# Kernel optimization log

Measured on AMD Instinct MI355X. Metric: run time of the kernel, lower is better.

## Reference

```python
import jax, jax.numpy as jnp
import numpy as np

T_STEPS, N, STATE, HID, ACT, C = 32, 64, 64, 128, 32, 96


def setup_inputs() -> dict:
    key = jax.random.key(0)
    ks = jax.random.split(key, 16)
    s = 0.05
    inp = {
        'x': jax.random.normal(ks[0], (T_STEPS, N, STATE), jnp.float32),
        'a': jax.random.normal(ks[1], (T_STEPS, N, ACT), jnp.float32),
        # GRU layer 0 (input state_dim) and layer 1 (input hidden_dim)
        'wih0': jax.random.normal(ks[2], (3 * HID, STATE), jnp.float32) * s,
        'whh0': jax.random.normal(ks[3], (3 * HID, HID), jnp.float32) * s,
        'bih0': jax.random.normal(ks[4], (3 * HID,), jnp.float32) * s,
        'bhh0': jax.random.normal(ks[5], (3 * HID,), jnp.float32) * s,
        'wih1': jax.random.normal(ks[6], (3 * HID, HID), jnp.float32) * s,
        'whh1': jax.random.normal(ks[7], (3 * HID, HID), jnp.float32) * s,
        'bih1': jax.random.normal(ks[8], (3 * HID,), jnp.float32) * s,
        'bhh1': jax.random.normal(ks[9], (3 * HID,), jnp.float32) * s,
        'w1': jax.random.normal(ks[10], (HID, HID + ACT), jnp.float32) * s,
        'b1': jax.random.normal(ks[11], (HID,), jnp.float32) * s,
        'w2': jax.random.normal(ks[12], (1, 2 * HID), jnp.float32) * s,
        'b2': jax.random.normal(ks[13], (1,), jnp.float32) * s,
        'Tm': jax.random.normal(ks[14], (HID, HID, C), jnp.float32),  # init.normal(T,0,1)
    }
    return inp


def _gru_cell(x_t, h, wih, whh, bih, bhh):
    gi = x_t @ wih.T + bih            # (N, 3H)
    gh = h @ whh.T + bhh
    i_r, i_z, i_n = jnp.split(gi, 3, axis=-1)
    h_r, h_z, h_n = jnp.split(gh, 3, axis=-1)
    r = jax.nn.sigmoid(i_r + h_r)
    z = jax.nn.sigmoid(i_z + h_z)
    n = jnp.tanh(i_n + r * h_n)
    return (1.0 - z) * n + z * h


def reference(x, a, wih0, whh0, bih0, bhh0, wih1, whh1, bih1, bhh1, w1, b1, w2, b2, Tm):
    def step(h, x_t):
        h0 = _gru_cell(x_t, h[0], wih0, whh0, bih0, bhh0)
        h1 = _gru_cell(h0, h[1], wih1, whh1, bih1, bhh1)
        return jnp.stack([h0, h1]), h1

    h_init = jnp.zeros((2, N, HID), x.dtype)
    _, p = jax.lax.scan(step, h_init, x)              # (T, N, H)

    fc1 = jax.nn.relu(jnp.concatenate([p, a], -1) @ w1.T + b1)  # (T, N, H)

    Tflat = Tm.reshape(HID, HID * C)

    def batch_discrim(xt):  # xt: (N, H)
        M = (xt @ Tflat).reshape(N, HID, C)           # (N, B, C)
        # pairwise L1 over C: (N, N, B)
        norm = jnp.abs(M[:, None] - M[None, :]).sum(-1)
        o_b = (jnp.exp(-norm).sum(0) - 1.0) / (N - 1)  # (N, B)
        return jnp.concatenate([xt, o_b], 1)          # (N, 2H)

    fc2 = jax.lax.map(batch_discrim, fc1)             # (T, N, 2H)
    prob = jax.nn.sigmoid(fc2 @ w2.T + b2)            # (T, N, 1)
    return prob
```

## Files before the change

### kernel.cpp

```cpp
#include <hip/hip_runtime.h>
#include <hip/hip_fp16.h>
#include <cstdint>

#define T_STEPS 32
#define NB 64
#define STATE 64
#define HID 128
#define ACT 32
#define CDIM 96
#define G3 (3*HID)

typedef __attribute__((ext_vector_type(8))) short short8;
typedef __attribute__((ext_vector_type(4))) float f32x4;
typedef _Float16 h2v __attribute__((ext_vector_type(2)));

__device__ __forceinline__ unsigned short f2bf(float f){
  unsigned int u = __builtin_bit_cast(unsigned int, f);
  u = u + 0x7FFFu + ((u >> 16) & 1u);
  return (unsigned short)(u >> 16);
}
__device__ __forceinline__ float bf2f(unsigned short u){
  unsigned int v = ((unsigned int)u) << 16; return __builtin_bit_cast(float, v);
}
__device__ __forceinline__ unsigned int packh2(float f0, float f1){
  return (unsigned int)__half_as_ushort(__float2half_rn(f0)) |
         ((unsigned int)__half_as_ushort(__float2half_rn(f1)) << 16);
}
__device__ __forceinline__ float sigmoidf_(float x){ return 1.0f/(1.0f + __expf(-x)); }
__device__ __forceinline__ float tanhf_(float x){ float e = __expf(2.0f*x); return (e-1.0f)/(e+1.0f); }

__device__ __forceinline__ float dot2f(float acc, unsigned int a, unsigned int b){
  h2v av = __builtin_bit_cast(h2v, a);
  h2v bv = __builtin_bit_cast(h2v, b);
  return __builtin_amdgcn_fdot2(av, bv, acc, false);
}
__device__ __forceinline__ float l1d(float acc, unsigned int ua, unsigned int ub){
  __half2 a = __builtin_bit_cast(__half2, ua);
  __half2 b = __builtin_bit_cast(__half2, ub);
  __half2 d = __habs2(__hsub2(a, b));
  h2v dv = __builtin_bit_cast(h2v, d);
  h2v ones; ones[0] = (_Float16)1.0f; ones[1] = (_Float16)1.0f;
  return __builtin_amdgcn_fdot2(dv, ones, acc, false);
}
__device__ __forceinline__ float l1d4(float acc, uint4 a, uint4 b){
  acc = l1d(acc, a.x, b.x); acc = l1d(acc, a.y, b.y);
  acc = l1d(acc, a.z, b.z); acc = l1d(acc, a.w, b.w);
  return acc;
}

__global__ void k_prep(const float* __restrict__ Tm, unsigned short* __restrict__ tmh,
                       const float* __restrict__ whh0, const float* __restrict__ whh1,
                       const float* __restrict__ w1, const float* __restrict__ wih0,
                       const float* __restrict__ wih1, const float* __restrict__ x,
                       const float* __restrict__ a,
                       unsigned int* __restrict__ whh0p, unsigned int* __restrict__ whh1p,
                       unsigned short* __restrict__ w1f, unsigned short* __restrict__ wi0f,
                       unsigned short* __restrict__ wi1f, unsigned short* __restrict__ xaf,
                       unsigned short* __restrict__ h1af){
  __shared__ __align__(4) unsigned short lt[12800];
  int tid = threadIdx.x;
  int bx = blockIdx.x;
  if (bx < 128){
    int b = bx;
    unsigned int* l2 = (unsigned int*)lt;
    for (int e4 = tid; e4 < 3072; e4 += 256){
      int k = e4 / 24, c4 = (e4 - k*24)*4;
      const float4 v = *(const float4*)(Tm + k*(HID*CDIM) + b*CDIM + c4);
      int base = (k*100 + c4) >> 1;
      l2[base]   = (unsigned int)f2bf(v.x) | ((unsigned int)f2bf(v.y) << 16);
      l2[base+1] = (unsigned int)f2bf(v.z) | ((unsigned int)f2bf(v.w) << 16);
    }
    __syncthreads();
    unsigned int* tm2 = (unsigned int*)(tmh + b*(HID*CDIM));
    for (int e2 = tid; e2 < 6144; e2 += 256){
      int e = e2*2;
      int chunk = e / 768;
      int r1 = e - chunk*768;
      int c = r1 >> 3, h = r1 & 7;
      unsigned int lo = lt[(chunk*8 + h)*100 + c];
      unsigned int hi = lt[(chunk*8 + h + 1)*100 + c];
      tm2[e2] = lo | (hi << 16);
    }
  } else if (bx < 132){
    for (int e = (bx-128)*256 + tid; e < 24576; e += 1024){
      int k2 = e / 384, r = e - k2*384;
      whh0p[e] = packh2(whh0[r*128 + 2*k2], whh0[r*128 + 2*k2 + 1]);
      whh1p[e] = packh2(whh1[r*128 + 2*k2], whh1[r*128 + 2*k2 + 1]);
    }
  } else if (bx < 136){
    for (int e = (bx-132)*256 + tid; e < 20480; e += 1024){
      int kc = e >> 10, rem = e & 1023;
      int col = rem >> 3, j = rem & 7;
      w1f[e] = f2bf(w1[col*160 + kc*8 + j]);
    }
  } else if (bx < 140){
    for (int e = (bx-136)*256 + tid; e < 24576; e += 1024){
      int kc = e / 3072, rem = e - kc*3072;
      int col = rem >> 3, kl = rem & 7;
      wi0f[e] = f2bf(wih0[col*64 + kc*8 + kl]);
    }
  } else if (bx < 144){
    for (int e = (bx-140)*256 + tid; e < 49152; e += 1024){
      int kc = e / 3072, rem = e - kc*3072;
      int col = rem >> 3, kl = rem & 7;
      wi1f[e] = f2bf(wih1[col*128 + kc*8 + kl]);
    }
  } else if (bx < 156){
    for (int e = (bx-144)*256 + tid; e < 131072; e += 3072){
      int t = e >> 12, rem = e & 4095;
      int ntile = rem >> 10, rem2 = rem & 1023;
      int kc = rem2 >> 7, nl = (rem2 >> 3) & 15, kl = rem2 & 7;
      int n = ntile*16 + nl, k = kc*8 + kl;
      xaf[e] = f2bf(x[t*4096 + n*64 + k]);
    }
  } else {
    for (int e = (bx-156)*256 + tid; e < 65536; e += 3072){
      int t = e >> 11, rem = e & 2047;
      int n = rem >> 5, c = rem & 31;
      int pos = t*10240 + (n>>4)*2560 + (16 + (c>>3))*128 + (n&15)*8 + (c&7);
      h1af[pos] = f2bf(a[t*(NB*ACT) + n*ACT + c]);
    }
  }
}

template<int KK, int TSU>
__global__ __launch_bounds__(256) void k_gi(const unsigned short* __restrict__ af,
                                            const unsigned short* __restrict__ wf,
                                            const float* __restrict__ bias,
                                            float* __restrict__ gig){
  int t = blockIdx.x, by = blockIdx.y, tid = threadIdx.x;
  int wave = tid >> 6, lane = tid & 63, m = lane & 15, quad = lane >> 4;
  const uint4* A4 = (const uint4*)af;
  const uint4* B4 = (const uint4*)wf;
  uint4 av[KK];
  #pragma unroll
  for (int kk = 0; kk < KK; kk++) av[kk] = A4[t*TSU + wave*(TSU/4) + (kk*4+quad)*16 + m];
  f32x4 acc[6];
  #pragma unroll
  for (int i = 0; i < 6; i++) acc[i] = (f32x4)(0.0f);
  #pragma unroll
  for (int kk = 0; kk < KK; kk++){
    short8 a = __builtin_bit_cast(short8, av[kk]);
    #pragma unroll
    for (int ntl = 0; ntl < 6; ntl++){
      int nt = by*6 + ntl;
      uint4 bv = B4[(kk*4+quad)*384 + nt*16 + m];
      acc[ntl] = __builtin_amdgcn_mfma_f32_16x16x32_bf16(a, __builtin_bit_cast(short8, bv), acc[ntl], 0, 0, 0);
    }
  }
  #pragma unroll
  for (int ntl = 0; ntl < 6; ntl++){
    int col = (by*6+ntl)*16 + m;
    float bv = bias[col];
    #pragma unroll
    for (int rr = 0; rr < 4; rr++){
      int n = wave*16 + quad*4 + rr;
      gig[(t*NB + n)*G3 + col] = acc[ntl][rr] + bv;
    }
  }
}

__global__ __launch_bounds__(768, 3) void k_rec2(const unsigned int* __restrict__ whh0p,
                                                 const unsigned int* __restrict__ whh1p,
                                                 const float* __restrict__ bhh0,
                                                 const float* __restrict__ bhh1,
                                                 const float* __restrict__ bih1,
                                                 const unsigned short* __restrict__ wi1f,
                                                 const float* __restrict__ gig,
                                                 unsigned short* __restrict__ h1af){
  __shared__ __align__(16) unsigned int hl[64];
  __shared__ float A0[G3];
  __shared__ __align__(16) float gl[T_STEPS*G3];
  __shared__ __align__(16) unsigned short hist0[T_STEPS*136];
  __shared__ __align__(16) unsigned short hist1[T_STEPS*HID];
  int n = blockIdx.x, tid = threadIdx.x;
  int r = tid >> 1, kh = tid & 1;
  {
    const float4* gg = (const float4*)gig;
    float4* gl4 = (float4*)gl;
    #pragma unroll
    for (int k = 0; k < 4; k++){
      int e = k*768 + tid;
      int t = e / 96, c = e - t*96;
      gl4[t*96 + c] = gg[(t*NB + n)*96 + c];
    }
  }
  unsigned int wh[32];
  #pragma unroll
  for (int i = 0; i < 32; i++) wh[i] = whh0p[(kh*32 + i)*384 + r];
  float bh = (kh == 0) ? bhh0[r] : 0.0f;
  if (tid < 64) hl[tid] = 0u;
  float hprev = 0.0f;
  __syncthreads();
  const uint4* h4 = (const uint4*)hl;
  for (int t = 0; t < T_STEPS; t++){
    float s0 = 0.0f, s1 = 0.0f, s2 = 0.0f, s3 = 0.0f;
    #pragma unroll
    for (int g = 0; g < 2; g++){
      uint4 hv[4];
      #pragma unroll
      for (int j = 0; j < 4; j++) hv[j] = h4[kh*8 + g*4 + j];
      s0 = dot2f(s0, wh[g*16 + 0], hv[0].x);  s0 = dot2f(s0, wh[g*16 + 1], hv[0].y);
      s0 = dot2f(s0, wh[g*16 + 2], hv[0].z);  s0 = dot2f(s0, wh[g*16 + 3], hv[0].w);
      s1 = dot2f(s1, wh[g*16 + 4], hv[1].x);  s1 = dot2f(s1, wh[g*16 + 5], hv[1].y);
      s1 = dot2f(s1, wh[g*16 + 6], hv[1].z);  s1 = dot2f(s1, wh[g*16 + 7], hv[1].w);
      s2 = dot2f(s2, wh[g*16 + 8], hv[2].x);  s2 = dot2f(s2, wh[g*16 + 9], hv[2].y);
      s2 = dot2f(s2, wh[g*16 +10], hv[2].z);  s2 = dot2f(s2, wh[g*16 +11], hv[2].w);
      s3 = dot2f(s3, wh[g*16 +12], hv[3].x);  s3 = dot2f(s3, wh[g*16 +13], hv[3].y);
      s3 = dot2f(s3, wh[g*16 +14], hv[3].z);  s3 = dot2f(s3, wh[g*16 +15], hv[3].w);
    }
    float gh = bh + ((s0 + s1) + (s2 + s3));
    gh += __shfl_xor(gh, 1);
    if (kh == 0) A0[r] = gh;
    __syncthreads();
    if (tid < HID){
      const float* gp = gl + t*G3;
      float rg = sigmoidf_(gp[tid]       + A0[tid]);
      float z  = sigmoidf_(gp[tid+HID]   + A0[tid+HID]);
      float nn = tanhf_   (gp[tid+2*HID] + rg*A0[tid+2*HID]);
      float hn = (1.0f - z)*nn + z*hprev;
      hprev = hn;
      ((__half*)hl)[tid] = __float2half_rn(hn);
      hist0[t*136 + tid] = f2bf(hn);
    }
    __syncthreads();
  }
  {
    int wave = tid >> 6, lane = tid & 63, m = lane & 15, quad = lane >> 4;
    const uint4* B4 = (const uint4*)wi1f;
    const uint4* H4 = (const uint4*)hist0;
    f32x4 acc00 = (f32x4)(0.0f), acc01 = (f32x4)(0.0f);
    f32x4 acc10 = (f32x4)(0.0f), acc11 = (f32x4)(0.0f);
    int nt0 = wave*2;
    #pragma unroll
    for (int kk = 0; kk < 4; kk++){
      uint4 a0 = H4[m*17 + kk*4 + quad];
      uint4 a1 = H4[(16 + m)*17 + kk*4 + quad];
      uint4 b0 = B4[(kk*4 + quad)*384 + nt0*16 + m];
      uint4 b1 = B4[(kk*4 + quad)*384 + (nt0+1)*16 + m];
      short8 a0s = __builtin_bit_cast(short8, a0);
      short8 a1s = __builtin_bit_cast(short8, a1);
      short8 b0s = __builtin_bit_cast(short8, b0);
      short8 b1s = __builtin_bit_cast(short8, b1);
      acc00 = __builtin_amdgcn_mfma_f32_16x16x32_bf16(a0s, b0s, acc00, 0, 0, 0);
      acc01 = __builtin_amdgcn_mfma_f32_16x16x32_bf16(a0s, b1s, acc01, 0, 0, 0);
      acc10 = __builtin_amdgcn_mfma_f32_16x16x32_bf16(a1s, b0s, acc10, 0, 0, 0);
      acc11 = __builtin_amdgcn_mfma_f32_16x16x32_bf16(a1s, b1s, acc11, 0, 0, 0);
    }
    float bv0 = bih1[nt0*16 + m];
    float bv1 = bih1[(nt0+1)*16 + m];
    #pragma unroll
    for (int rr = 0; rr < 4; rr++){
      gl[(quad*4 + rr)*G3 + nt0*16 + m]        = acc00[rr] + bv0;
      gl[(quad*4 + rr)*G3 + (nt0+1)*16 + m]    = acc01[rr] + bv1;
      gl[(16 + quad*4 + rr)*G3 + nt0*16 + m]   = acc10[rr] + bv0;
      gl[(16 + quad*4 + rr)*G3 + (nt0+1)*16 + m] = acc11[rr] + bv1;
    }
  }
  asm volatile("" ::: "memory");
  #pragma unroll
  for (int i = 0; i < 32; i++) wh[i] = whh1p[(kh*32 + i)*384 + r];
  bh = (kh == 0) ? bhh1[r] : 0.0f;
  if (tid < 64) hl[tid] = 0u;
  hprev = 0.0f;
  __syncthreads();
  for (int t = 0; t < T_STEPS; t++){
    float s0 = 0.0f, s1 = 0.0f, s2 = 0.0f, s3 = 0.0f;
    #pragma unroll
    for (int g = 0; g < 2; g++){
      uint4 hv[4];
      #pragma unroll
      for (int j = 0; j < 4; j++) hv[j] = h4[kh*8 + g*4 + j];
      s0 = dot2f(s0, wh[g*16 + 0], hv[0].x);  s0 = dot2f(s0, wh[g*16 + 1], hv[0].y);
      s0 = dot2f(s0, wh[g*16 + 2], hv[0].z);  s0 = dot2f(s0, wh[g*16 + 3], hv[0].w);
      s1 = dot2f(s1, wh[g*16 + 4], hv[1].x);  s1 = dot2f(s1, wh[g*16 + 5], hv[1].y);
      s1 = dot2f(s1, wh[g*16 + 6], hv[1].z);  s1 = dot2f(s1, wh[g*16 + 7], hv[1].w);
      s2 = dot2f(s2, wh[g*16 + 8], hv[2].x);  s2 = dot2f(s2, wh[g*16 + 9], hv[2].y);
      s2 = dot2f(s2, wh[g*16 +10], hv[2].z);  s2 = dot2f(s2, wh[g*16 +11], hv[2].w);
      s3 = dot2f(s3, wh[g*16 +12], hv[3].x);  s3 = dot2f(s3, wh[g*16 +13], hv[3].y);
      s3 = dot2f(s3, wh[g*16 +14], hv[3].z);  s3 = dot2f(s3, wh[g*16 +15], hv[3].w);
    }
    float gh = bh + ((s0 + s1) + (s2 + s3));
    gh += __shfl_xor(gh, 1);
    if (kh == 0) A0[r] = gh;
    __syncthreads();
    if (tid < HID){
      const float* gp = gl + t*G3;
      float rg = sigmoidf_(gp[tid]       + A0[tid]);
      float z  = sigmoidf_(gp[tid+HID]   + A0[tid+HID]);
      float nn = tanhf_   (gp[tid+2*HID] + rg*A0[tid+2*HID]);
      float hn = (1.0f - z)*nn + z*hprev;
      hprev = hn;
      ((__half*)hl)[tid] = __float2half_rn(hn);
      hist1[t*HID + tid] = f2bf(hn);
    }
    __syncthreads();
  }
  if (tid < T_STEPS*16){
    int t = tid >> 4, j = tid & 15;
    uint4 v = *(const uint4*)(hist1 + t*HID + j*8);
    *(uint4*)(h1af + t*10240 + (n>>4)*2560 + j*128 + (n&15)*8) = v;
  }
}

__global__ __launch_bounds__(256) void k_fc1(const unsigned short* __restrict__ h1af,
                                             const unsigned short* __restrict__ w1f,
                                             const float* __restrict__ b1,
                                             unsigned short* __restrict__ fc1h){
  __shared__ float b1s[128];
  int t = blockIdx.x, tid = threadIdx.x;
  int wave = tid >> 6, lane = tid & 63, m = lane & 15, quad = lane >> 4;
  if (tid < 128) b1s[tid] = b1[tid];
  const uint4* A4 = (const uint4*)(h1af + t*10240);
  const uint4* B4 = (const uint4*)w1f;
  f32x4 acc[8];
  #pragma unroll
  for (int i = 0; i < 8; i++) acc[i] = (f32x4)(0.0f);
  #pragma unroll
  for (int ks = 0; ks < 5; ks++){
    uint4 av = A4[wave*320 + (ks*4 + quad)*16 + m];
    short8 avs = __builtin_bit_cast(short8, av);
    #pragma unroll
    for (int nt = 0; nt < 8; nt++){
      uint4 bv = B4[(ks*4 + quad)*128 + nt*16 + m];
      acc[nt] = __builtin_amdgcn_mfma_f32_16x16x32_bf16(avs, __builtin_bit_cast(short8, bv), acc[nt], 0, 0, 0);
    }
  }
  __syncthreads();
  #pragma unroll
  for (int nt = 0; nt < 8; nt++){
    float bj = b1s[nt*16 + m];
    #pragma unroll
    for (int rr = 0; rr < 4; rr++){
      float v = fmaxf(acc[nt][rr] + bj, 0.0f);
      fc1h[t*8192 + wave*2048 + (nt*2 + (m>>3))*128 + (quad*4 + rr)*8 + (m&7)] = f2bf(v);
    }
  }
}

__global__ __launch_bounds__(256) void k_disc(const unsigned short* __restrict__ fc1h,
                                              const unsigned short* __restrict__ tmh,
                                              float* __restrict__ O){
  __shared__ __align__(16) __half Mh[64*120];
  __shared__ unsigned short plist[2016];
  __shared__ float osum[64];
  __shared__ unsigned int cnt;
  int b = blockIdx.x, t = blockIdx.y;
  int tid = threadIdx.x;
  int wave = tid >> 6, lane = tid & 63, m = lane & 15, quad = lane >> 4;
  if (tid < 64) osum[tid] = 0.0f;
  if (tid == 0) cnt = 0u;
  const uint4* Bg = (const uint4*)(tmh + b*(CDIM*HID));
  const uint4* Ag = (const uint4*)(fc1h + t*8192);
  uint4 a4[4];
  #pragma unroll
  for (int kk = 0; kk < 4; kk++) a4[kk] = Ag[wave*256 + (kk*4 + quad)*16 + m];
  f32x4 acc[6];
  #pragma unroll
  for (int i = 0; i < 6; i++) acc[i] = (f32x4)(0.0f);
  #pragma unroll
  for (int kk = 0; kk < 4; kk++){
    short8 av = __builtin_bit_cast(short8, a4[kk]);
    #pragma unroll
    for (int nt = 0; nt < 6; nt++){
      uint4 b4 = Bg[(kk*4 + quad)*96 + nt*16 + m];
      acc[nt] = __builtin_amdgcn_mfma_f32_16x16x32_bf16(av, __builtin_bit_cast(short8, b4), acc[nt], 0, 0, 0);
    }
  }
  #pragma unroll
  for (int nt = 0; nt < 6; nt++){
    #pragma unroll
    for (int rr = 0; rr < 4; rr++){
      Mh[(wave*16 + quad*4 + rr)*120 + nt*16 + m] = __float2half(acc[nt][rr]);
    }
  }
  __syncthreads();
  const unsigned int ONES2 = 0x3C003C00u;
  #pragma unroll
  for (int idx = tid; idx < 512; idx += 256){
    int r = idx >> 3, jc = idx & 7;
    const unsigned int* row = (const unsigned int*)(Mh + r*120 + jc*12);
    float s = 0.0f;
    #pragma unroll
    for (int q = 0; q < 6; q++) s = dot2f(s, row[q], ONES2);
    Mh[r*120 + 96 + jc] = __float2half(s);
  }
  __syncthreads();
  const uint4* M4 = (const uint4*)Mh;
  for (int p = tid; p < 2016; p += 256){
    int r = p >> 5, s = p & 31;
    int i, j;
    if (s == 0){ i = 63; j = r; }
    else {
      i = r + s;      if (i >= 63) i -= 63;
      j = r + 63 - s; if (j >= 63) j -= 63;
    }
    uint4 qa = M4[i*15 + 12];
    uint4 qb = M4[j*15 + 12];
    float lb = l1d4(0.0f, qa, qb);
    if (lb <= 14.5f){
      unsigned int k = atomicAdd(&cnt, 1u);
      plist[k] = (unsigned short)(i*64 + j);
    }
  }
  __syncthreads();
  int ns = (int)cnt;
  if (ns > 2016) ns = 2016;
  for (int v = tid; v < ns; v += 256){
    int pr = plist[v];
    int i = pr >> 6, j = pr & 63;
    float L = 0.0f;
    #pragma unroll
    for (int c = 0; c < 12; c++){
      L = l1d4(L, M4[i*15 + c], M4[j*15 + c]);
    }
    float e = __expf(-L);
    atomicAdd(&osum[i], e);
    atomicAdd(&osum[j], e);
  }
  __syncthreads();
  if (tid < 64) O[(t*HID + b)*NB + tid] = osum[tid]*(1.0f/63.0f);
}

__global__ __launch_bounds__(256) void k_final(const unsigned short* __restrict__ fc1h,
                                               const float* __restrict__ O,
                                               const float* __restrict__ w2, const float* __restrict__ b2,
                                               float* __restrict__ out){
  __shared__ float ol[NB*HID];
  __shared__ unsigned short fr[8192];
  __shared__ float wl[2*HID + 2];
  __shared__ float pp[4][NB];
  int t = blockIdx.x, tid = threadIdx.x;
  for (int i = tid; i < NB*HID; i += 256) ol[i] = O[t*NB*HID + i];
  const uint4* Fg = (const uint4*)(fc1h + t*8192);
  for (int i = tid; i < 1024; i += 256) ((uint4*)fr)[i] = Fg[i];
  if (tid < 2*HID) wl[tid] = w2[tid];
  if (tid == 0) wl[2*HID] = b2[0];
  __syncthreads();
  int n = tid & 63, part = tid >> 6;
  float acc = 0.0f;
  int base = (n>>4)*2048 + (n&15)*8;
  #pragma unroll
  for (int jc = 0; jc < 4; jc++){
    int j8 = part*4 + jc;
    #pragma unroll
    for (int k = 0; k < 8; k++)
      acc += bf2f(fr[base + j8*128 + k])*wl[j8*8 + k];
  }
  #pragma unroll 8
  for (int bb = 0; bb < 32; bb++){
    int bq = part*32 + bb;
    acc += ol[bq*NB + n]*wl[HID + bq];
  }
  pp[part][n] = acc;
  __syncthreads();
  if (tid < NB){
    float s = wl[2*HID] + pp[0][tid] + pp[1][tid] + pp[2][tid] + pp[3][tid];
    out[t*NB + tid] = sigmoidf_(s);
  }
}

extern "C" void kernel_launch(void* const* d_in, const int* in_sizes, int n_in,
                              void* d_out, int out_size, void* d_ws, size_t ws_size,
                              hipStream_t stream){
  const float* x    = (const float*)d_in[0];
  const float* a    = (const float*)d_in[1];
  const float* wih0 = (const float*)d_in[2];
  const float* whh0 = (const float*)d_in[3];
  const float* bih0 = (const float*)d_in[4];
  const float* bhh0 = (const float*)d_in[5];
  const float* wih1 = (const float*)d_in[6];
  const float* whh1 = (const float*)d_in[7];
  const float* bih1 = (const float*)d_in[8];
  const float* bhh1 = (const float*)d_in[9];
  const float* w1   = (const float*)d_in[10];
  const float* b1   = (const float*)d_in[11];
  const float* w2   = (const float*)d_in[12];
  const float* b2   = (const float*)d_in[13];
  const float* Tm   = (const float*)d_in[14];
  float* ws = (float*)d_ws;
  float* Ows = ws;
  unsigned int* whh0p = (unsigned int*)(ws + 262144);
  unsigned int* whh1p = (unsigned int*)(ws + 286720);
  unsigned short* tmh  = (unsigned short*)(ws + 311296);
  unsigned short* fc1h = (unsigned short*)(ws + 1097728);
  unsigned short* h1af = (unsigned short*)(ws + 1228800);
  unsigned short* w1f  = (unsigned short*)(ws + 1392640);
  unsigned short* xaf  = (unsigned short*)(ws + 1402880);
  unsigned short* wi0f = (unsigned short*)(ws + 1468416);
  unsigned short* wi1f = (unsigned short*)(ws + 1480704);
  float* gig = ws + 1636352;
  float* out = (float*)d_out;

  k_prep<<<dim3(168), dim3(256), 0, stream>>>(Tm, tmh, whh0, whh1, w1, wih0, wih1, x, a,
                                              whh0p, whh1p, w1f, wi0f, wi1f, xaf, h1af);
  k_gi<2, 512><<<dim3(T_STEPS, 4), dim3(256), 0, stream>>>(xaf, wi0f, bih0, gig);
  k_rec2<<<dim3(NB), dim3(768), 0, stream>>>(whh0p, whh1p, bhh0, bhh1, bih1, wi1f, gig, h1af);
  k_fc1<<<dim3(T_STEPS), dim3(256), 0, stream>>>(h1af, w1f, b1, fc1h);
  k_disc<<<dim3(HID, T_STEPS), dim3(256), 0, stream>>>(fc1h, tmh, Ows);
  k_final<<<dim3(T_STEPS), dim3(256), 0, stream>>>(fc1h, Ows, w2, b2, out);
}
```

Measured before the change: 180.4 us.

## Interleave two batch rows per recurrent block to overlap matvec and gate phases

The recurrent GRU kernel now handles two batch rows per block and software-pipelines them. In each barrier interval the block computes the hidden matvec for one row while the first 128 threads apply the gate nonlinearities for the other row. This is meant to hide the serial gate phase and halve the barriers per step pair. In exchange it doubles shared memory per block, launches half as many blocks (32 instead of 64), and lowers the occupancy hint to 1. The serial chain per block becomes longer.

```diff
diff --git a/kernel.cpp b/kernel.cpp
--- a/kernel.cpp
+++ b/kernel.cpp
@@ -160,7 +160,7 @@
   }
 }
 
-__global__ __launch_bounds__(768, 3) void k_rec2(const unsigned int* __restrict__ whh0p,
+__global__ __launch_bounds__(768, 1) void k_rec2(const unsigned int* __restrict__ whh0p,
                                                  const unsigned int* __restrict__ whh1p,
                                                  const float* __restrict__ bhh0,
                                                  const float* __restrict__ bhh1,
@@ -168,137 +168,155 @@
                                                  const unsigned short* __restrict__ wi1f,
                                                  const float* __restrict__ gig,
                                                  unsigned short* __restrict__ h1af){
-  __shared__ __align__(16) unsigned int hl[64];
-  __shared__ float A0[G3];
-  __shared__ __align__(16) float gl[T_STEPS*G3];
-  __shared__ __align__(16) unsigned short hist0[T_STEPS*136];
-  __shared__ __align__(16) unsigned short hist1[T_STEPS*HID];
-  int n = blockIdx.x, tid = threadIdx.x;
+  __shared__ __align__(16) unsigned int hl[2][64];
+  __shared__ float A0[2][G3];
+  __shared__ __align__(16) float gl[2][T_STEPS*G3];
+  __shared__ __align__(16) unsigned short hist0[2][T_STEPS*136];
+  __shared__ __align__(16) unsigned short hist1[2][T_STEPS*HID];
+  int n0 = blockIdx.x*2, tid = threadIdx.x;
   int r = tid >> 1, kh = tid & 1;
   {
     const float4* gg = (const float4*)gig;
     float4* gl4 = (float4*)gl;
     #pragma unroll
-    for (int k = 0; k < 4; k++){
+    for (int k = 0; k < 8; k++){
       int e = k*768 + tid;
-      int t = e / 96, c = e - t*96;
-      gl4[t*96 + c] = gg[(t*NB + n)*96 + c];
+      int s = e / 3072, rem = e - s*3072;
+      int t = rem / 96, c = rem - t*96;
+      gl4[s*3072 + t*96 + c] = gg[(t*NB + n0 + s)*96 + c];
     }
   }
   unsigned int wh[32];
   #pragma unroll
   for (int i = 0; i < 32; i++) wh[i] = whh0p[(kh*32 + i)*384 + r];
   float bh = (kh == 0) ? bhh0[r] : 0.0f;
-  if (tid < 64) hl[tid] = 0u;
-  float hprev = 0.0f;
-  __syncthreads();
-  const uint4* h4 = (const uint4*)hl;
-  for (int t = 0; t < T_STEPS; t++){
-    float s0 = 0.0f, s1 = 0.0f, s2 = 0.0f, s3 = 0.0f;
-    #pragma unroll
-    for (int g = 0; g < 2; g++){
-      uint4 hv[4];
+  if (tid < 128) ((unsigned int*)hl)[tid] = 0u;
+  float hp0 = 0.0f, hp1 = 0.0f;
+  __syncthreads();
+  for (int i = 0; i <= 2*T_STEPS; i++){
+    int s = i & 1, ts = i >> 1;
+    if (ts < T_STEPS){
+      const uint4* h4s = (const uint4*)(hl[s]);
+      float s0 = 0.0f, s1 = 0.0f, s2 = 0.0f, s3 = 0.0f;
       #pragma unroll
-      for (int j = 0; j < 4; j++) hv[j] = h4[kh*8 + g*4 + j];
-      s0 = dot2f(s0, wh[g*16 + 0], hv[0].x);  s0 = dot2f(s0, wh[g*16 + 1], hv[0].y);
-      s0 = dot2f(s0, wh[g*16 + 2], hv[0].z);  s0 = dot2f(s0, wh[g*16 + 3], hv[0].w);
-      s1 = dot2f(s1, wh[g*16 + 4], hv[1].x);  s1 = dot2f(s1, wh[g*16 + 5], hv[1].y);
-      s1 = dot2f(s1, wh[g*16 + 6], hv[1].z);  s1 = dot2f(s1, wh[g*16 + 7], hv[1].w);
-      s2 = dot2f(s2, wh[g*16 + 8], hv[2].x);  s2 = dot2f(s2, wh[g*16 + 9], hv[2].y);
-      s2 = dot2f(s2, wh[g*16 +10], hv[2].z);  s2 = dot2f(s2, wh[g*16 +11], hv[2].w);
-      s3 = dot2f(s3, wh[g*16 +12], hv[3].x);  s3 = dot2f(s3, wh[g*16 +13], hv[3].y);
-      s3 = dot2f(s3, wh[g*16 +14], hv[3].z);  s3 = dot2f(s3, wh[g*16 +15], hv[3].w);
-    }
-    float gh = bh + ((s0 + s1) + (s2 + s3));
-    gh += __shfl_xor(gh, 1);
-    if (kh == 0) A0[r] = gh;
-    __syncthreads();
-    if (tid < HID){
-      const float* gp = gl + t*G3;
-      float rg = sigmoidf_(gp[tid]       + A0[tid]);
-      float z  = sigmoidf_(gp[tid+HID]   + A0[tid+HID]);
-      float nn = tanhf_   (gp[tid+2*HID] + rg*A0[tid+2*HID]);
-      float hn = (1.0f - z)*nn + z*hprev;
-      hprev = hn;
-      ((__half*)hl)[tid] = __float2half_rn(hn);
-      hist0[t*136 + tid] = f2bf(hn);
+      for (int g = 0; g < 2; g++){
+        uint4 hv[4];
+        #pragma unroll
+        for (int j = 0; j < 4; j++) hv[j] = h4s[kh*8 + g*4 + j];
+        s0 = dot2f(s0, wh[g*16 + 0], hv[0].x);  s0 = dot2f(s0, wh[g*16 + 1], hv[0].y);
+        s0 = dot2f(s0, wh[g*16 + 2], hv[0].z);  s0 = dot2f(s0, wh[g*16 + 3], hv[0].w);
+        s1 = dot2f(s1, wh[g*16 + 4], hv[1].x);  s1 = dot2f(s1, wh[g*16 + 5], hv[1].y);
+        s1 = dot2f(s1, wh[g*16 + 6], hv[1].z);  s1 = dot2f(s1, wh[g*16 + 7], hv[1].w);
+        s2 = dot2f(s2, wh[g*16 + 8], hv[2].x);  s2 = dot2f(s2, wh[g*16 + 9], hv[2].y);
+        s2 = dot2f(s2, wh[g*16 +10], hv[2].z);  s2 = dot2f(s2, wh[g*16 +11], hv[2].w);
+        s3 = dot2f(s3, wh[g*16 +12], hv[3].x);  s3 = dot2f(s3, wh[g*16 +13], hv[3].y);
+        s3 = dot2f(s3, wh[g*16 +14], hv[3].z);  s3 = dot2f(s3, wh[g*16 +15], hv[3].w);
+      }
+      float gh = bh + ((s0 + s1) + (s2 + s3));
+      gh += __shfl_xor(gh, 1);
+      if (kh == 0) A0[s][r] = gh;
+    }
+    int so = s ^ 1, to = (i - 1) >> 1;
+    if (i >= 1 && to < T_STEPS && tid < HID){
+      const float* gp = gl[so] + to*G3;
+      const float* ap = A0[so];
+      float rg = sigmoidf_(gp[tid]       + ap[tid]);
+      float z  = sigmoidf_(gp[tid+HID]   + ap[tid+HID]);
+      float nn = tanhf_   (gp[tid+2*HID] + rg*ap[tid+2*HID]);
+      float hp = so ? hp1 : hp0;
+      float hn = (1.0f - z)*nn + z*hp;
+      if (so) hp1 = hn; else hp0 = hn;
+      ((__half*)(hl[so]))[tid] = __float2half_rn(hn);
+      hist0[so][to*136 + tid] = f2bf(hn);
     }
     __syncthreads();
   }
   {
     int wave = tid >> 6, lane = tid & 63, m = lane & 15, quad = lane >> 4;
     const uint4* B4 = (const uint4*)wi1f;
-    const uint4* H4 = (const uint4*)hist0;
-    f32x4 acc00 = (f32x4)(0.0f), acc01 = (f32x4)(0.0f);
-    f32x4 acc10 = (f32x4)(0.0f), acc11 = (f32x4)(0.0f);
     int nt0 = wave*2;
-    #pragma unroll
-    for (int kk = 0; kk < 4; kk++){
-      uint4 a0 = H4[m*17 + kk*4 + quad];
-      uint4 a1 = H4[(16 + m)*17 + kk*4 + quad];
-      uint4 b0 = B4[(kk*4 + quad)*384 + nt0*16 + m];
-      uint4 b1 = B4[(kk*4 + quad)*384 + (nt0+1)*16 + m];
-      short8 a0s = __builtin_bit_cast(short8, a0);
-      short8 a1s = __builtin_bit_cast(short8, a1);
-      short8 b0s = __builtin_bit_cast(short8, b0);
-      short8 b1s = __builtin_bit_cast(short8, b1);
-      acc00 = __builtin_amdgcn_mfma_f32_16x16x32_bf16(a0s, b0s, acc00, 0, 0, 0);
-      acc01 = __builtin_amdgcn_mfma_f32_16x16x32_bf16(a0s, b1s, acc01, 0, 0, 0);
-      acc10 = __builtin_amdgcn_mfma_f32_16x16x32_bf16(a1s, b0s, acc10, 0, 0, 0);
-      acc11 = __builtin_amdgcn_mfma_f32_16x16x32_bf16(a1s, b1s, acc11, 0, 0, 0);
-    }
     float bv0 = bih1[nt0*16 + m];
     float bv1 = bih1[(nt0+1)*16 + m];
     #pragma unroll
-    for (int rr = 0; rr < 4; rr++){
-      gl[(quad*4 + rr)*G3 + nt0*16 + m]        = acc00[rr] + bv0;
-      gl[(quad*4 + rr)*G3 + (nt0+1)*16 + m]    = acc01[rr] + bv1;
-      gl[(16 + quad*4 + rr)*G3 + nt0*16 + m]   = acc10[rr] + bv0;
-      gl[(16 + quad*4 + rr)*G3 + (nt0+1)*16 + m] = acc11[rr] + bv1;
+    for (int s = 0; s < 2; s++){
+      const uint4* H4 = (const uint4*)(hist0[s]);
+      f32x4 acc00 = (f32x4)(0.0f), acc01 = (f32x4)(0.0f);
+      f32x4 acc10 = (f32x4)(0.0f), acc11 = (f32x4)(0.0f);
+      #pragma unroll
+      for (int kk = 0; kk < 4; kk++){
+        uint4 a0 = H4[m*17 + kk*4 + quad];
+        uint4 a1 = H4[(16 + m)*17 + kk*4 + quad];
+        uint4 b0 = B4[(kk*4 + quad)*384 + nt0*16 + m];
+        uint4 b1 = B4[(kk*4 + quad)*384 + (nt0+1)*16 + m];
+        short8 a0s = __builtin_bit_cast(short8, a0);
+        short8 a1s = __builtin_bit_cast(short8, a1);
+        short8 b0s = __builtin_bit_cast(short8, b0);
+        short8 b1s = __builtin_bit_cast(short8, b1);
+        acc00 = __builtin_amdgcn_mfma_f32_16x16x32_bf16(a0s, b0s, acc00, 0, 0, 0);
+        acc01 = __builtin_amdgcn_mfma_f32_16x16x32_bf16(a0s, b1s, acc01, 0, 0, 0);
+        acc10 = __builtin_amdgcn_mfma_f32_16x16x32_bf16(a1s, b0s, acc10, 0, 0, 0);
+        acc11 = __builtin_amdgcn_mfma_f32_16x16x32_bf16(a1s, b1s, acc11, 0, 0, 0);
+      }
+      float* gls = gl[s];
+      #pragma unroll
+      for (int rr = 0; rr < 4; rr++){
+        gls[(quad*4 + rr)*G3 + nt0*16 + m]          = acc00[rr] + bv0;
+        gls[(quad*4 + rr)*G3 + (nt0+1)*16 + m]      = acc01[rr] + bv1;
+        gls[(16 + quad*4 + rr)*G3 + nt0*16 + m]     = acc10[rr] + bv0;
+        gls[(16 + quad*4 + rr)*G3 + (nt0+1)*16 + m] = acc11[rr] + bv1;
+      }
     }
   }
   asm volatile("" ::: "memory");
   #pragma unroll
   for (int i = 0; i < 32; i++) wh[i] = whh1p[(kh*32 + i)*384 + r];
   bh = (kh == 0) ? bhh1[r] : 0.0f;
-  if (tid < 64) hl[tid] = 0u;
-  hprev = 0.0f;
-  __syncthreads();
-  for (int t = 0; t < T_STEPS; t++){
-    float s0 = 0.0f, s1 = 0.0f, s2 = 0.0f, s3 = 0.0f;
-    #pragma unroll
-    for (int g = 0; g < 2; g++){
-      uint4 hv[4];
+  if (tid < 128) ((unsigned int*)hl)[tid] = 0u;
+  hp0 = 0.0f; hp1 = 0.0f;
+  __syncthreads();
+  for (int i = 0; i <= 2*T_STEPS; i++){
+    int s = i & 1, ts = i >> 1;
+    if (ts < T_STEPS){
+      const uint4* h4s = (const uint4*)(hl[s]);
+      float s0 = 0.0f, s1 = 0.0f, s2 = 0.0f, s3 = 0.0f;
       #pragma unroll
-      for (int j = 0; j < 4; j++) hv[j] = h4[kh*8 + g*4 + j];
-      s0 = dot2f(s0, wh[g*16 + 0], hv[0].x);  s0 = dot2f(s0, wh[g*16 + 1], hv[0].y);
-      s0 = dot2f(s0, wh[g*16 + 2], hv[0].z);  s0 = dot2f(s0, wh[g*16 + 3], hv[0].w);
-      s1 = dot2f(s1, wh[g*16 + 4], hv[1].x);  s1 = dot2f(s1, wh[g*16 + 5], hv[1].y);
-      s1 = dot2f(s1, wh[g*16 + 6], hv[1].z);  s1 = dot2f(s1, wh[g*16 + 7], hv[1].w);
-      s2 = dot2f(s2, wh[g*16 + 8], hv[2].x);  s2 = dot2f(s2, wh[g*16 + 9], hv[2].y);
-      s2 = dot2f(s2, wh[g*16 +10], hv[2].z);  s2 = dot2f(s2, wh[g*16 +11], hv[2].w);
-      s3 = dot2f(s3, wh[g*16 +12], hv[3].x);  s3 = dot2f(s3, wh[g*16 +13], hv[3].y);
-      s3 = dot2f(s3, wh[g*16 +14], hv[3].z);  s3 = dot2f(s3, wh[g*16 +15], hv[3].w);
-    }
-    float gh = bh + ((s0 + s1) + (s2 + s3));
-    gh += __shfl_xor(gh, 1);
-    if (kh == 0) A0[r] = gh;
+      for (int g = 0; g < 2; g++){
+        uint4 hv[4];
+        #pragma unroll
+        for (int j = 0; j < 4; j++) hv[j] = h4s[kh*8 + g*4 + j];
+        s0 = dot2f(s0, wh[g*16 + 0], hv[0].x);  s0 = dot2f(s0, wh[g*16 + 1], hv[0].y);
+        s0 = dot2f(s0, wh[g*16 + 2], hv[0].z);  s0 = dot2f(s0, wh[g*16 + 3], hv[0].w);
+        s1 = dot2f(s1, wh[g*16 + 4], hv[1].x);  s1 = dot2f(s1, wh[g*16 + 5], hv[1].y);
+        s1 = dot2f(s1, wh[g*16 + 6], hv[1].z);  s1 = dot2f(s1, wh[g*16 + 7], hv[1].w);
+        s2 = dot2f(s2, wh[g*16 + 8], hv[2].x);  s2 = dot2f(s2, wh[g*16 + 9], hv[2].y);
+        s2 = dot2f(s2, wh[g*16 +10], hv[2].z);  s2 = dot2f(s2, wh[g*16 +11], hv[2].w);
+        s3 = dot2f(s3, wh[g*16 +12], hv[3].x);  s3 = dot2f(s3, wh[g*16 +13], hv[3].y);
+        s3 = dot2f(s3, wh[g*16 +14], hv[3].z);  s3 = dot2f(s3, wh[g*16 +15], hv[3].w);
+      }
+      float gh = bh + ((s0 + s1) + (s2 + s3));
+      gh += __shfl_xor(gh, 1);
+      if (kh == 0) A0[s][r] = gh;
+    }
+    int so = s ^ 1, to = (i - 1) >> 1;
+    if (i >= 1 && to < T_STEPS && tid < HID){
+      const float* gp = gl[so] + to*G3;
+      const float* ap = A0[so];
+      float rg = sigmoidf_(gp[tid]       + ap[tid]);
+      float z  = sigmoidf_(gp[tid+HID]   + ap[tid+HID]);
+      float nn = tanhf_   (gp[tid+2*HID] + rg*ap[tid+2*HID]);
+      float hp = so ? hp1 : hp0;
+      float hn = (1.0f - z)*nn + z*hp;
+      if (so) hp1 = hn; else hp0 = hn;
+      ((__half*)(hl[so]))[tid] = __float2half_rn(hn);
+      hist1[so][to*HID + tid] = f2bf(hn);
+    }
     __syncthreads();
-    if (tid < HID){
-      const float* gp = gl + t*G3;
-      float rg = sigmoidf_(gp[tid]       + A0[tid]);
-      float z  = sigmoidf_(gp[tid+HID]   + A0[tid+HID]);
-      float nn = tanhf_   (gp[tid+2*HID] + rg*A0[tid+2*HID]);
-      float hn = (1.0f - z)*nn + z*hprev;
-      hprev = hn;
-      ((__half*)hl)[tid] = __float2half_rn(hn);
-      hist1[t*HID + tid] = f2bf(hn);
-    }
-    __syncthreads();
-  }
-  if (tid < T_STEPS*16){
-    int t = tid >> 4, j = tid & 15;
-    uint4 v = *(const uint4*)(hist1 + t*HID + j*8);
+  }
+  for (int e = tid; e < 2*T_STEPS*16; e += 768){
+    int s = e >> 9, rem = e & 511;
+    int t = rem >> 4, j = rem & 15;
+    int n = n0 + s;
+    uint4 v = *(const uint4*)(hist1[s] + t*HID + j*8);
     *(uint4*)(h1af + t*10240 + (n>>4)*2560 + j*128 + (n&15)*8) = v;
   }
 }
@@ -495,7 +513,7 @@
   k_prep<<<dim3(168), dim3(256), 0, stream>>>(Tm, tmh, whh0, whh1, w1, wih0, wih1, x, a,
                                               whh0p, whh1p, w1f, wi0f, wi1f, xaf, h1af);
   k_gi<2, 512><<<dim3(T_STEPS, 4), dim3(256), 0, stream>>>(xaf, wi0f, bih0, gig);
-  k_rec2<<<dim3(NB), dim3(768), 0, stream>>>(whh0p, whh1p, bhh0, bhh1, bih1, wi1f, gig, h1af);
+  k_rec2<<<dim3(NB/2), dim3(768), 0, stream>>>(whh0p, whh1p, bhh0, bhh1, bih1, wi1f, gig, h1af);
   k_fc1<<<dim3(T_STEPS), dim3(256), 0, stream>>>(h1af, w1f, b1, fc1h);
   k_disc<<<dim3(HID, T_STEPS), dim3(256), 0, stream>>>(fc1h, tmh, Ows);
   k_final<<<dim3(T_STEPS), dim3(256), 0, stream>>>(fc1h, Ows, w2, b2, out);
```

Measured after the change: 207.5 us. +15.1%, slower.

## Fuse layer-0 input projection GEMM into recurrent kernel prologue

Applied to the files above, without the earlier changes.

Drops the separate k_gi launch that computed x@wih0^T+bih0 for all timesteps into a global float buffer. Each recurrent block now computes its own batch row's 32x384 input-gate tile with MFMA directly into shared memory, reading x in a new per-batch bf16 layout. This removes a kernel launch and the global write and read-back of the gate buffer. In exchange, the serial recurrent kernel does this GEMM in its prologue, and each block reads the whole wih0 weight matrix.

```diff
diff --git a/kernel.cpp b/kernel.cpp
--- a/kernel.cpp
+++ b/kernel.cpp
@@ -55,7 +55,7 @@
                        const float* __restrict__ a,
                        unsigned int* __restrict__ whh0p, unsigned int* __restrict__ whh1p,
                        unsigned short* __restrict__ w1f, unsigned short* __restrict__ wi0f,
-                       unsigned short* __restrict__ wi1f, unsigned short* __restrict__ xaf,
+                       unsigned short* __restrict__ wi1f, unsigned short* __restrict__ xnf,
                        unsigned short* __restrict__ h1af){
   __shared__ __align__(4) unsigned short lt[12800];
   int tid = threadIdx.x;
@@ -107,11 +107,9 @@
     }
   } else if (bx < 156){
     for (int e = (bx-144)*256 + tid; e < 131072; e += 3072){
-      int t = e >> 12, rem = e & 4095;
-      int ntile = rem >> 10, rem2 = rem & 1023;
-      int kc = rem2 >> 7, nl = (rem2 >> 3) & 15, kl = rem2 & 7;
-      int n = ntile*16 + nl, k = kc*8 + kl;
-      xaf[e] = f2bf(x[t*4096 + n*64 + k]);
+      int n = e >> 11, rem = e & 2047;
+      int t = rem >> 6, k = rem & 63;
+      xnf[e] = f2bf(x[t*4096 + n*64 + k]);
     }
   } else {
     for (int e = (bx-156)*256 + tid; e < 65536; e += 3072){
@@ -123,50 +121,15 @@
   }
 }
 
-template<int KK, int TSU>
-__global__ __launch_bounds__(256) void k_gi(const unsigned short* __restrict__ af,
-                                            const unsigned short* __restrict__ wf,
-                                            const float* __restrict__ bias,
-                                            float* __restrict__ gig){
-  int t = blockIdx.x, by = blockIdx.y, tid = threadIdx.x;
-  int wave = tid >> 6, lane = tid & 63, m = lane & 15, quad = lane >> 4;
-  const uint4* A4 = (const uint4*)af;
-  const uint4* B4 = (const uint4*)wf;
-  uint4 av[KK];
-  #pragma unroll
-  for (int kk = 0; kk < KK; kk++) av[kk] = A4[t*TSU + wave*(TSU/4) + (kk*4+quad)*16 + m];
-  f32x4 acc[6];
-  #pragma unroll
-  for (int i = 0; i < 6; i++) acc[i] = (f32x4)(0.0f);
-  #pragma unroll
-  for (int kk = 0; kk < KK; kk++){
-    short8 a = __builtin_bit_cast(short8, av[kk]);
-    #pragma unroll
-    for (int ntl = 0; ntl < 6; ntl++){
-      int nt = by*6 + ntl;
-      uint4 bv = B4[(kk*4+quad)*384 + nt*16 + m];
-      acc[ntl] = __builtin_amdgcn_mfma_f32_16x16x32_bf16(a, __builtin_bit_cast(short8, bv), acc[ntl], 0, 0, 0);
-    }
-  }
-  #pragma unroll
-  for (int ntl = 0; ntl < 6; ntl++){
-    int col = (by*6+ntl)*16 + m;
-    float bv = bias[col];
-    #pragma unroll
-    for (int rr = 0; rr < 4; rr++){
-      int n = wave*16 + quad*4 + rr;
-      gig[(t*NB + n)*G3 + col] = acc[ntl][rr] + bv;
-    }
-  }
-}
-
 __global__ __launch_bounds__(768, 3) void k_rec2(const unsigned int* __restrict__ whh0p,
                                                  const unsigned int* __restrict__ whh1p,
                                                  const float* __restrict__ bhh0,
                                                  const float* __restrict__ bhh1,
+                                                 const float* __restrict__ bih0,
                                                  const float* __restrict__ bih1,
+                                                 const unsigned short* __restrict__ wi0f,
                                                  const unsigned short* __restrict__ wi1f,
-                                                 const float* __restrict__ gig,
+                                                 const unsigned short* __restrict__ xnf,
                                                  unsigned short* __restrict__ h1af){
   __shared__ __align__(16) unsigned int hl[64];
   __shared__ float A0[G3];
@@ -176,13 +139,35 @@
   int n = blockIdx.x, tid = threadIdx.x;
   int r = tid >> 1, kh = tid & 1;
   {
-    const float4* gg = (const float4*)gig;
-    float4* gl4 = (float4*)gl;
-    #pragma unroll
-    for (int k = 0; k < 4; k++){
-      int e = k*768 + tid;
-      int t = e / 96, c = e - t*96;
-      gl4[t*96 + c] = gg[(t*NB + n)*96 + c];
+    int wave = tid >> 6, lane = tid & 63, m = lane & 15, quad = lane >> 4;
+    const uint4* B4 = (const uint4*)wi0f;
+    const uint4* X4 = (const uint4*)(xnf + n*2048);
+    f32x4 acc00 = (f32x4)(0.0f), acc01 = (f32x4)(0.0f);
+    f32x4 acc10 = (f32x4)(0.0f), acc11 = (f32x4)(0.0f);
+    int nt0 = wave*2;
+    #pragma unroll
+    for (int kk = 0; kk < 2; kk++){
+      uint4 a0 = X4[m*8 + kk*4 + quad];
+      uint4 a1 = X4[(16 + m)*8 + kk*4 + quad];
+      uint4 b0 = B4[(kk*4 + quad)*384 + nt0*16 + m];
+      uint4 b1 = B4[(kk*4 + quad)*384 + (nt0+1)*16 + m];
+      short8 a0s = __builtin_bit_cast(short8, a0);
+      short8 a1s = __builtin_bit_cast(short8, a1);
+      short8 b0s = __builtin_bit_cast(short8, b0);
+      short8 b1s = __builtin_bit_cast(short8, b1);
+      acc00 = __builtin_amdgcn_mfma_f32_16x16x32_bf16(a0s, b0s, acc00, 0, 0, 0);
+      acc01 = __builtin_amdgcn_mfma_f32_16x16x32_bf16(a0s, b1s, acc01, 0, 0, 0);
+      acc10 = __builtin_amdgcn_mfma_f32_16x16x32_bf16(a1s, b0s, acc10, 0, 0, 0);
+      acc11 = __builtin_amdgcn_mfma_f32_16x16x32_bf16(a1s, b1s, acc11, 0, 0, 0);
+    }
+    float bv0 = bih0[nt0*16 + m];
+    float bv1 = bih0[(nt0+1)*16 + m];
+    #pragma unroll
+    for (int rr = 0; rr < 4; rr++){
+      gl[(quad*4 + rr)*G3 + nt0*16 + m]          = acc00[rr] + bv0;
+      gl[(quad*4 + rr)*G3 + (nt0+1)*16 + m]      = acc01[rr] + bv1;
+      gl[(16 + quad*4 + rr)*G3 + nt0*16 + m]     = acc10[rr] + bv0;
+      gl[(16 + quad*4 + rr)*G3 + (nt0+1)*16 + m] = acc11[rr] + bv1;
     }
   }
   unsigned int wh[32];
@@ -486,16 +471,15 @@
   unsigned short* fc1h = (unsigned short*)(ws + 1097728);
   unsigned short* h1af = (unsigned short*)(ws + 1228800);
   unsigned short* w1f  = (unsigned short*)(ws + 1392640);
-  unsigned short* xaf  = (unsigned short*)(ws + 1402880);
+  unsigned short* xnf  = (unsigned short*)(ws + 1402880);
   unsigned short* wi0f = (unsigned short*)(ws + 1468416);
   unsigned short* wi1f = (unsigned short*)(ws + 1480704);
-  float* gig = ws + 1636352;
   float* out = (float*)d_out;
 
   k_prep<<<dim3(168), dim3(256), 0, stream>>>(Tm, tmh, whh0, whh1, w1, wih0, wih1, x, a,
-                                              whh0p, whh1p, w1f, wi0f, wi1f, xaf, h1af);
-  k_gi<2, 512><<<dim3(T_STEPS, 4), dim3(256), 0, stream>>>(xaf, wi0f, bih0, gig);
-  k_rec2<<<dim3(NB), dim3(768), 0, stream>>>(whh0p, whh1p, bhh0, bhh1, bih1, wi1f, gig, h1af);
+                                              whh0p, whh1p, w1f, wi0f, wi1f, xnf, h1af);
+  k_rec2<<<dim3(NB), dim3(768), 0, stream>>>(whh0p, whh1p, bhh0, bhh1, bih0, bih1,
+                                             wi0f, wi1f, xnf, h1af);
   k_fc1<<<dim3(T_STEPS), dim3(256), 0, stream>>>(h1af, w1f, b1, fc1h);
   k_disc<<<dim3(HID, T_STEPS), dim3(256), 0, stream>>>(fc1h, tmh, Ows);
   k_final<<<dim3(T_STEPS), dim3(256), 0, stream>>>(fc1h, Ows, w2, b2, out);
```

New measurement: 176.8 us (median of 2 runs). 2.0% less time.
